# Kernel optimization log

Measured on AMD Instinct MI355X. Metric: run time of the kernel, lower is better.

## Reference

```python
import jax, jax.numpy as jnp
import numpy as np

L, B, N, D, H, DH, MLP = 4, 4, 2048, 512, 8, 64, 2048
EPS = 1e-5


def layer_norm(x, w, b):
    mu = jnp.mean(x, axis=-1, keepdims=True)
    var = jnp.mean(jnp.square(x - mu), axis=-1, keepdims=True)
    return (x - mu) * jax.lax.rsqrt(var + EPS) * w + b


def setup_inputs() -> dict:
    key = jax.random.key(0)
    ks = jax.random.split(key, 8)
    x = jax.random.normal(ks[0], (B, N, D), dtype=jnp.float32)
    # mask == 1.0 means blocked: triu(ones) - eye -> strict upper triangle
    mask = jnp.triu(jnp.ones((N, N), dtype=jnp.float32)) - jnp.eye(N, dtype=jnp.float32)
    s = 0.02
    return {
        "x": x,
        "mask": mask,
        "ln1_w": jnp.ones((L, D), jnp.float32),
        "ln1_b": jnp.zeros((L, D), jnp.float32),
        "w_qkv": jax.random.normal(ks[1], (L, D, 3 * H * DH), jnp.float32) * s,
        "w_out": jax.random.normal(ks[2], (L, H * DH, D), jnp.float32) * s,
        "b_out": jnp.zeros((L, D), jnp.float32),
        "ln2_w": jnp.ones((L, D), jnp.float32),
        "ln2_b": jnp.zeros((L, D), jnp.float32),
        "w1": jax.random.normal(ks[3], (L, D, MLP), jnp.float32) * s,
        "b1": jnp.zeros((L, MLP), jnp.float32),
        "w2": jax.random.normal(ks[4], (L, MLP, D), jnp.float32) * s,
        "b2": jnp.zeros((L, D), jnp.float32),
    }


def reference(x, mask, ln1_w, ln1_b, w_qkv, w_out, b_out, ln2_w, ln2_b, w1, b1, w2, b2):
    scale = DH ** (-0.5)
    blocked = (mask == 1.0)  # [N, N]
    for l in range(L):
        # --- masked self-attention (pre-norm) ---
        h = layer_norm(x, ln1_w[l], ln1_b[l])
        qkv = h @ w_qkv[l]                               # [B, N, 3*H*DH]
        q, k, v = jnp.split(qkv, 3, axis=-1)
        q = q.reshape(B, N, H, DH).transpose(0, 2, 1, 3)  # bhnd
        k = k.reshape(B, N, H, DH).transpose(0, 2, 1, 3)
        v = v.reshape(B, N, H, DH).transpose(0, 2, 1, 3)
        scores = jnp.einsum('bhnd,bhmd->bhnm', q, k) * scale
        scores = jnp.where(blocked, -jnp.inf, scores)
        att = jax.nn.softmax(scores, axis=-1)
        o = jnp.einsum('bhnm,bhmd->bhnd', att, v)
        o = o.transpose(0, 2, 1, 3).reshape(B, N, H * DH)
        x = x + (o @ w_out[l] + b_out[l])
        # --- GELU MLP (pre-norm) ---
        h2 = layer_norm(x, ln2_w[l], ln2_b[l])
        ff = jax.nn.gelu(h2 @ w1[l] + b1[l], approximate=False) @ w2[l] + b2[l]
        x = x + ff
    return x
```

## Files before the change

### kernel.cpp

```cpp
#include <hip/hip_runtime.h>
#include <math.h>

#define L 4
#define BATCH 4
#define N 2048
#define D 512
#define H 8
#define DH 64
#define MLPD 2048
#define M_ROWS (BATCH * N)
#define VTP 2064

using v8s = __attribute__((ext_vector_type(8))) short;
using v4f = __attribute__((ext_vector_type(4))) float;

__device__ inline short f2bf(float f) {
  union { float f; unsigned u; } v; v.f = f;
  unsigned r = v.u + 0x7FFFu + ((v.u >> 16) & 1u);
  return (short)(r >> 16);
}
__device__ inline unsigned pack2bf_t(float a, float b) {
  union { float f; unsigned u; } x, y; x.f = a; y.f = b;
  return (x.u >> 16) | (y.u & 0xFFFF0000u);
}

#define MFMA(a, b, c) __builtin_amdgcn_mfma_f32_16x16x32_bf16(a, b, c, 0, 0, 0)

__device__ __forceinline__ void gload_lds16(const void* g, void* l) {
  __builtin_amdgcn_global_load_lds((const __attribute__((address_space(1))) void*)g,
                                   (__attribute__((address_space(3))) void*)l, 16, 0, 0);
}

#define FENCE asm volatile("" ::: "memory")
#define BAR  do { FENCE; __builtin_amdgcn_s_barrier(); FENCE; } while (0)
#define VMW(n) asm volatile("s_waitcnt vmcnt(" #n ")" ::: "memory")

__global__ void copyf4_kernel(const float4* __restrict__ in, float4* __restrict__ out, int n) {
  int i = blockIdx.x * blockDim.x + threadIdx.x;
  if (i < n) out[i] = in[i];
}

__launch_bounds__(256)
__global__ void transpose_w_kernel(const float* __restrict__ src, short* __restrict__ dst,
                                   int R, int C) {
  __shared__ float tile[32][33];
  const size_t base = (size_t)blockIdx.z * R * C;
  const int c0 = blockIdx.x * 32, r0 = blockIdx.y * 32;
  const int tx = threadIdx.x & 31, ty = threadIdx.x >> 5;
  #pragma unroll
  for (int i = ty; i < 32; i += 8)
    tile[i][tx] = src[base + (size_t)(r0 + i) * C + c0 + tx];
  __syncthreads();
  #pragma unroll
  for (int i = ty; i < 32; i += 8)
    dst[base + (size_t)(c0 + i) * R + r0 + tx] = f2bf(tile[tx][i]);
}

__launch_bounds__(256)
__global__ void ln_kernel(const float* __restrict__ x, const float* __restrict__ w,
                          const float* __restrict__ b, short* __restrict__ out) {
  const int row = blockIdx.x * 4 + (threadIdx.x >> 6);
  const int lane = threadIdx.x & 63;
  const float* xr = x + (size_t)row * D;
  float4 a0 = *(const float4*)(xr + lane * 8);
  float4 a1 = *(const float4*)(xr + lane * 8 + 4);
  float v[8] = {a0.x, a0.y, a0.z, a0.w, a1.x, a1.y, a1.z, a1.w};
  float s = 0.f;
  #pragma unroll
  for (int j = 0; j < 8; ++j) s += v[j];
  #pragma unroll
  for (int m = 1; m < 64; m <<= 1) s += __shfl_xor(s, m, 64);
  const float mean = s * (1.0f / D);
  float q = 0.f;
  #pragma unroll
  for (int j = 0; j < 8; ++j) { float d = v[j] - mean; q += d * d; }
  #pragma unroll
  for (int m = 1; m < 64; m <<= 1) q += __shfl_xor(q, m, 64);
  const float rstd = rsqrtf(q * (1.0f / D) + 1e-5f);
  float4 w0 = *(const float4*)(w + lane * 8);
  float4 w1 = *(const float4*)(w + lane * 8 + 4);
  float4 b0 = *(const float4*)(b + lane * 8);
  float4 b1 = *(const float4*)(b + lane * 8 + 4);
  float wv[8] = {w0.x, w0.y, w0.z, w0.w, w1.x, w1.y, w1.z, w1.w};
  float bv[8] = {b0.x, b0.y, b0.z, b0.w, b1.x, b1.y, b1.z, b1.w};
  v8s r;
  #pragma unroll
  for (int j = 0; j < 8; ++j) r[j] = f2bf((v[j] - mean) * rstd * wv[j] + bv[j]);
  *(v8s*)(out + (size_t)row * D + lane * 8) = r;
}

template <int MODE, int NT>
__launch_bounds__(512, 2)
__global__ void gemm256_kernel(const short* __restrict__ A, const short* __restrict__ Bt,
                               const float* __restrict__ bias, void* __restrict__ Out,
                               int M, int Nc) {
  constexpr int K = NT * 64;
  __shared__ __align__(16) short Ah[4][128 * 64];
  __shared__ __align__(16) short Bh[4][128 * 64];
  const int tid = threadIdx.x, lane = tid & 63, w = tid >> 6;
  const int wr = w >> 2, wc = w & 3;
  const int r16 = lane & 15, g = lane >> 4;

  const int nxb = Nc >> 8;
  const int nyb = M >> 8;
  const int bid = (int)blockIdx.x;
  const int xcd = bid & 7, ii = bid >> 3;
  const int byi = xcd * (nyb >> 3) + ii / nxb;
  const int bxi = ii % nxb;
  const int m0 = byi << 8, n0 = bxi << 8;

  const int srow = lane >> 3;
  const int ssw = ((lane & 7) ^ srow) * 8;

  const short* Abase = A + (size_t)(m0 + srow) * K + ssw;
  const short* Bbase = Bt + (size_t)(n0 + srow) * K + ssw;

  auto STAGE_A = [&](int j) {
    if (j >= 2 * NT) return;
    const int slot = j & 3, k0 = (j >> 1) * 64, r0 = (j & 1) * 128;
    #pragma unroll
    for (int i = 0; i < 2; ++i) {
      const int rr = i * 64 + w * 8;
      gload_lds16(Abase + (size_t)(r0 + rr) * K + k0, (char*)&Ah[slot][0] + rr * 128);
    }
  };
  auto STAGE_B = [&](int j) {
    if (j >= 2 * NT) return;
    const int slot = j & 3, k0 = (j >> 1) * 64, c0 = (j & 1) * 128;
    #pragma unroll
    for (int i = 0; i < 2; ++i) {
      const int rr = i * 64 + w * 8;
      gload_lds16(Bbase + (size_t)(c0 + rr) * K + k0, (char*)&Bh[slot][0] + rr * 128);
    }
  };

  const int arow = wr * 64 + r16;
  const int brow = wc * 32 + r16;
  const int swz7 = r16 & 7;

  v8s ar[4][2], br0[2][2], br1[2][2];
  auto LDA = [&](int slot) {
    const char* base = (const char*)&Ah[slot][0];
    #pragma unroll
    for (int mf = 0; mf < 4; ++mf)
      #pragma unroll
      for (int kh = 0; kh < 2; ++kh)
        ar[mf][kh] = *(const v8s*)(base + (arow + mf * 16) * 128 + (((kh * 4 + g) ^ swz7) * 16));
  };
  auto LDB0 = [&](int slot) {
    const char* base = (const char*)&Bh[slot][0];
    #pragma unroll
    for (int nf = 0; nf < 2; ++nf)
      #pragma unroll
      for (int kh = 0; kh < 2; ++kh)
        br0[nf][kh] = *(const v8s*)(base + (brow + nf * 16) * 128 + (((kh * 4 + g) ^ swz7) * 16));
  };
  auto LDB1 = [&](int slot) {
    const char* base = (const char*)&Bh[slot][0];
    #pragma unroll
    for (int nf = 0; nf < 2; ++nf)
      #pragma unroll
      for (int kh = 0; kh < 2; ++kh)
        br1[nf][kh] = *(const v8s*)(base + (brow + nf * 16) * 128 + (((kh * 4 + g) ^ swz7) * 16));
  };

  v4f acc[2][2][4][2] = {};

#define MMA_Q(QM, QN, BR)                                                      \
  do {                                                                         \
    __builtin_amdgcn_s_setprio(1);                                             \
    _Pragma("unroll")                                                          \
    for (int kh = 0; kh < 2; ++kh)                                             \
      _Pragma("unroll")                                                        \
      for (int mf = 0; mf < 4; ++mf)                                           \
        _Pragma("unroll")                                                      \
        for (int nf = 0; nf < 2; ++nf)                                         \
          acc[QM][QN][mf][nf] = MFMA(ar[mf][kh], BR[nf][kh], acc[QM][QN][mf][nf]); \
    __builtin_amdgcn_s_setprio(0);                                             \
  } while (0)

  STAGE_A(0); STAGE_B(0); STAGE_B(1); STAGE_A(1); STAGE_A(2); STAGE_B(2); STAGE_B(3);
  VMW(6);
  BAR;

  auto KTILE = [&](int T, int sa) {
    LDA(sa); LDB0(sa);
    STAGE_A(2 * T + 3);
    BAR;
    MMA_Q(0, 0, br0);
    BAR;
    LDB1(sa + 1);
    BAR;
    MMA_Q(0, 1, br1);
    BAR;
    LDA(sa + 1);
    STAGE_A(2 * T + 4); STAGE_B(2 * T + 4);
    BAR;
    MMA_Q(1, 1, br1);
    BAR;
    STAGE_B(2 * T + 5);
    BAR;
    MMA_Q(1, 0, br0);
    VMW(4);
    BAR;
  };

  #pragma unroll
  for (int t2 = 0; t2 < NT / 2; ++t2) {
    KTILE(2 * t2, 0);
    KTILE(2 * t2 + 1, 2);
  }
#undef MMA_Q

  #pragma unroll
  for (int qm = 0; qm < 2; ++qm)
    #pragma unroll
    for (int mf = 0; mf < 4; ++mf) {
      const int row = m0 + qm * 128 + wr * 64 + mf * 16 + g * 4;
      #pragma unroll
      for (int qn = 0; qn < 2; ++qn)
        #pragma unroll
        for (int nf = 0; nf < 2; ++nf) {
          const int col = n0 + qn * 128 + wc * 32 + nf * 16 + r16;
          float bv = 0.0f;
          if constexpr (MODE == 1) bv = bias[col];
          #pragma unroll
          for (int r = 0; r < 4; ++r) {
            float val = acc[qm][qn][mf][nf][r] + bv;
            if constexpr (MODE == 1) {
              const float z = val * 0.70710678118f;
              const float az = fabsf(z);
              const float t = 1.0f / (1.0f + 0.3275911f * az);
              const float p =
                  0.254829592f +
                  t * (-0.284496736f + t * (1.421413741f + t * (-1.453152027f + t * 1.061405429f)));
              float er = 1.0f - p * t * __expf(-az * az);
              er = (z < 0.0f) ? -er : er;
              val = 0.5f * val * (1.0f + er);
            }
            ((short*)Out)[(size_t)(row + r) * Nc + col] = f2bf(val);
          }
        }
    }
}

template <int MODE, int BN>
__launch_bounds__(256)
__global__ void gemm128_kernel(const short* __restrict__ A, const short* __restrict__ Bt,
                               const float* __restrict__ bias, const float* __restrict__ Xres,
                               void* __restrict__ Out, int M, int Nc, int K) {
  constexpr int MR = (BN == 128) ? 4 : 2;
  __shared__ __align__(16) short As[2][128 * 64];
  __shared__ __align__(16) short Bs[2][BN * 64];
  const int tid = threadIdx.x;
  const int lane = tid & 63;
  const int w = tid >> 6;
  const int wr = (BN == 128) ? (w >> 1) : w;
  const int wc = (BN == 128) ? (w & 1) : 0;
  const int r16 = lane & 15, g = lane >> 4;

  const int nxb = Nc / BN;
  const int nyb = M >> 7;
  const int bid = (int)blockIdx.x;
  const int xcd = bid & 7;
  const int ii = bid >> 3;
  const int byi = xcd * (nyb >> 3) + ii / nxb;
  const int bxi = ii % nxb;
  const int m0 = byi * 128, n0 = bxi * BN;

  const int srow = lane >> 3;
  const int ssw = ((lane & 7) ^ srow) * 8;

  auto STAGE = [&](int buf, int k0) {
    #pragma unroll
    for (int j = 0; j < 4; ++j) {
      const int row = w * 32 + j * 8;
      gload_lds16(A + (size_t)(m0 + row + srow) * K + k0 + ssw,
                  (char*)&As[buf][0] + row * 128);
    }
    #pragma unroll
    for (int j = 0; j < BN / 32; ++j) {
      const int row = w * (BN / 4) + j * 8;
      gload_lds16(Bt + (size_t)(n0 + row + srow) * K + k0 + ssw,
                  (char*)&Bs[buf][0] + row * 128);
    }
  };

  v4f acc[MR][4] = {};

  STAGE(0, 0);
  __syncthreads();
  int cur = 0;
  for (int k0 = 0; k0 < K; k0 += 64) {
    if (k0 + 64 < K) STAGE(cur ^ 1, k0 + 64);
    v8s af[MR][2], bf[4][2];
    #pragma unroll
    for (int m = 0; m < MR; ++m) {
      const int row = wr * (MR * 16) + m * 16 + r16;
      #pragma unroll
      for (int kh = 0; kh < 2; ++kh)
        af[m][kh] = *(const v8s*)((const char*)&As[cur][0] + row * 128 +
                                  (((kh * 4 + g) ^ (row & 7)) * 16));
    }
    #pragma unroll
    for (int n = 0; n < 4; ++n) {
      const int row = wc * 64 + n * 16 + r16;
      #pragma unroll
      for (int kh = 0; kh < 2; ++kh)
        bf[n][kh] = *(const v8s*)((const char*)&Bs[cur][0] + row * 128 +
                                  (((kh * 4 + g) ^ (row & 7)) * 16));
    }
    #pragma unroll
    for (int kh = 0; kh < 2; ++kh)
      #pragma unroll
      for (int m = 0; m < MR; ++m)
        #pragma unroll
        for (int n = 0; n < 4; ++n)
          acc[m][n] = MFMA(af[m][kh], bf[n][kh], acc[m][n]);
    __syncthreads();
    cur ^= 1;
  }

  #pragma unroll
  for (int m = 0; m < MR; ++m) {
    const int row = m0 + wr * (MR * 16) + m * 16 + g * 4;
    #pragma unroll
    for (int n = 0; n < 4; ++n) {
      const int col = n0 + wc * 64 + n * 16 + r16;
      const float bv = bias ? bias[col] : 0.0f;
      #pragma unroll
      for (int r = 0; r < 4; ++r) {
        const size_t idx = (size_t)(row + r) * Nc + col;
        float val = acc[m][n][r] + bv;
        if constexpr (MODE == 0) {
          ((short*)Out)[idx] = f2bf(val);
        } else if constexpr (MODE == 1) {
          const float z = val * 0.70710678118f;
          const float az = fabsf(z);
          const float t = 1.0f / (1.0f + 0.3275911f * az);
          const float p =
              0.254829592f +
              t * (-0.284496736f + t * (1.421413741f + t * (-1.453152027f + t * 1.061405429f)));
          float er = 1.0f - p * t * __expf(-az * az);
          er = (z < 0.0f) ? -er : er;
          val = 0.5f * val * (1.0f + er);
          ((short*)Out)[idx] = f2bf(val);
        } else {
          ((float*)Out)[idx] = val + Xres[idx];
        }
      }
    }
  }
}

__launch_bounds__(256)
__global__ void kv_prep_kernel(const short* __restrict__ qkv, short* __restrict__ Vt) {
  __shared__ __align__(16) short tile[64][88];
  const int b = blockIdx.z, h = blockIdx.y, n0 = blockIdx.x * 64;
  const int tid = threadIdx.x;
  const int bh = b * H + h;
  const int row2 = tid >> 3, d0 = (tid & 7) * 8;
  #pragma unroll
  for (int i = 0; i < 2; ++i) {
    const int n = i * 32 + row2;
    const short* src = qkv + ((size_t)(b * N + n0 + n)) * 1536 + 1024 + h * 64 + d0;
    *(v8s*)&tile[n][d0] = *(const v8s*)src;
  }
  __syncthreads();
  const int dh = tid & 63, nc = (tid >> 6) * 16;
  #pragma unroll
  for (int j = 0; j < 2; ++j) {
    const int oc = nc + j * 8;
    const int base = (oc >> 5) * 32 + ((oc >> 3) & 3) * 4;
    v8s ov;
    #pragma unroll
    for (int e = 0; e < 4; ++e) ov[e] = tile[base + e][dh];
    #pragma unroll
    for (int e = 0; e < 4; ++e) ov[4 + e] = tile[base + 16 + e][dh];
    *(v8s*)(Vt + ((size_t)(bh * 64 + dh)) * VTP + n0 + oc) = ov;
  }
}

__launch_bounds__(256)
__global__ void attn_kernel(const short* __restrict__ qkv, const short* __restrict__ Vt,
                            short* __restrict__ o) {
  __shared__ __align__(16) short Ks[2][64 * 64];
  __shared__ __align__(16) short Vs[2][64 * 64];
  const int lin = (int)blockIdx.x;
  const int bh = ((lin >> 3) & 3) * 8 + (lin & 7);
  const int xl2 = 31 - (lin >> 5);
  const int b = bh >> 3, h = bh & 7;
  const int q0 = xl2 * 64;
  const int tid = threadIdx.x, lane = tid & 63, w = tid >> 6;
  const int r16 = lane & 15, g = lane >> 4;
  const int qw = q0 + w * 16;

  v8s qf0, qf1;
  {
    const size_t qbase = ((size_t)(b * N + qw + r16)) * 1536 + h * 64;
    qf0 = *(const v8s*)(qkv + qbase + g * 8);
    qf1 = *(const v8s*)(qkv + qbase + 32 + g * 8);
  }

  const short* vtb = Vt + (size_t)bh * 64 * VTP;

  const int srow = lane >> 3;
  const int ssw = ((lane & 7) ^ srow) * 8;

  v4f oacc[4] = {};
  float lsum = 0.f;
  const int tdiag = xl2;

  auto STAGE = [&](int buf, int t) {
    const int k0 = t * 64;
    #pragma unroll
    for (int j = 0; j < 2; ++j) {
      const int row = w * 16 + j * 8 + srow;
      gload_lds16(qkv + ((size_t)(b * N + k0 + row)) * 1536 + 512 + h * 64 + ssw,
                  (char*)&Ks[buf][0] + (w * 16 + j * 8) * 128);
      gload_lds16(vtb + (size_t)row * VTP + k0 + ssw,
                  (char*)&Vs[buf][0] + (w * 16 + j * 8) * 128);
    }
  };

  STAGE(0, 0);
  __syncthreads();
  int cur = 0;
  for (int t = 0; t <= tdiag; ++t) {
    if (t < tdiag) STAGE(cur ^ 1, t + 1);
    const int k0 = t * 64;
    const char* kb = (const char*)&Ks[cur][0];
    const char* vb = (const char*)&Vs[cur][0];

    v8s vf[4][2];
    #pragma unroll
    for (int a = 0; a < 4; ++a)
      #pragma unroll
      for (int c = 0; c < 2; ++c)
        vf[a][c] = *(const v8s*)(vb + (a * 16 + r16) * 128 + (((c * 4 + g) ^ (r16 & 7)) * 16));

    __builtin_amdgcn_s_setprio(1);
    v4f s[4];
    #pragma unroll
    for (int kt = 0; kt < 4; ++kt) {
      const int krow = (kt * 16 + r16) * 128;
      v8s kfa = *(const v8s*)(kb + krow + ((g ^ (r16 & 7)) * 16));
      v8s kfb = *(const v8s*)(kb + krow + (((4 + g) ^ (r16 & 7)) * 16));
      v4f ss = {};
      ss = MFMA(kfa, qf0, ss);
      ss = MFMA(kfb, qf1, ss);
      s[kt] = ss;
    }
    __builtin_amdgcn_s_setprio(0);

    const bool needmask = (t == tdiag);
    const int qrow = qw + r16;
    const int kbase = k0 + 4 * g;
    unsigned pw_[8];
    #pragma unroll
    for (int kt = 0; kt < 4; ++kt) {
      float e[4];
      #pragma unroll
      for (int r = 0; r < 4; ++r) {
        float v = s[kt][r] * 0.125f;
        if (needmask && (kbase + kt * 16 + r > qrow)) v = -3e38f;
        e[r] = __expf(v);
      }
      lsum += (e[0] + e[1]) + (e[2] + e[3]);
      pw_[kt * 2 + 0] = pack2bf_t(e[0], e[1]);
      pw_[kt * 2 + 1] = pack2bf_t(e[2], e[3]);
    }
    union PU { unsigned u[4]; v8s s8; };
    PU pa0, pa1;
    pa0.u[0] = pw_[0]; pa0.u[1] = pw_[1]; pa0.u[2] = pw_[2]; pa0.u[3] = pw_[3];
    pa1.u[0] = pw_[4]; pa1.u[1] = pw_[5]; pa1.u[2] = pw_[6]; pa1.u[3] = pw_[7];

    __builtin_amdgcn_s_setprio(1);
    #pragma unroll
    for (int dt = 0; dt < 4; ++dt) oacc[dt] = MFMA(pa0.s8, vf[dt][0], oacc[dt]);
    #pragma unroll
    for (int dt = 0; dt < 4; ++dt) oacc[dt] = MFMA(pa1.s8, vf[dt][1], oacc[dt]);
    __builtin_amdgcn_s_setprio(0);

    __syncthreads();
    cur ^= 1;
  }

  lsum += __shfl_xor(lsum, 16, 64);
  lsum += __shfl_xor(lsum, 32, 64);
  float ldiv[4];
  #pragma unroll
  for (int r = 0; r < 4; ++r) ldiv[r] = __shfl(lsum, g * 4 + r, 64);

  #pragma unroll
  for (int dt = 0; dt < 4; ++dt)
    #pragma unroll
    for (int r = 0; r < 4; ++r) {
      const float val = oacc[dt][r] / ldiv[r];
      o[((size_t)(b * N + qw + g * 4 + r)) * 512 + h * 64 + dt * 16 + r16] = f2bf(val);
    }
}

extern "C" void kernel_launch(void* const* d_in, const int* in_sizes, int n_in,
                              void* d_out, int out_size, void* d_ws, size_t ws_size,
                              hipStream_t stream) {
  const float* x_in  = (const float*)d_in[0];
  const float* ln1_w = (const float*)d_in[2];
  const float* ln1_b = (const float*)d_in[3];
  const float* w_qkv = (const float*)d_in[4];
  const float* w_out = (const float*)d_in[5];
  const float* b_out = (const float*)d_in[6];
  const float* ln2_w = (const float*)d_in[7];
  const float* ln2_b = (const float*)d_in[8];
  const float* w1    = (const float*)d_in[9];
  const float* b1    = (const float*)d_in[10];
  const float* w2    = (const float*)d_in[11];
  const float* b2    = (const float*)d_in[12];

  char* ws = (char*)d_ws;
  size_t off = 0;
  auto alloc = [&](size_t bytes) { char* p = ws + off; off += (bytes + 255) & ~(size_t)255; return p; };
  short* wqkvT = (short*)alloc((size_t)L * 1536 * 512 * 2);
  short* woutT = (short*)alloc((size_t)L * 512 * 512 * 2);
  short* w1T   = (short*)alloc((size_t)L * 512 * 2048 * 2);
  short* w2T   = (short*)alloc((size_t)L * 2048 * 512 * 2);
  short* hln   = (short*)alloc((size_t)M_ROWS * 512 * 2);
  short* big   = (short*)alloc((size_t)M_ROWS * 2048 * 2);
  short* oatt  = (short*)alloc((size_t)M_ROWS * 512 * 2);
  short* Vtg   = (short*)alloc((size_t)BATCH * H * 64 * VTP * 2);
  short* qkv = big;
  short* ff  = big;

  float* x = (float*)d_out;

  copyf4_kernel<<<4096, 256, 0, stream>>>((const float4*)x_in, (float4*)x, M_ROWS * D / 4);

  transpose_w_kernel<<<dim3(1536 / 32, 512 / 32, L), 256, 0, stream>>>(w_qkv, wqkvT, 512, 1536);
  transpose_w_kernel<<<dim3(512 / 32, 512 / 32, L), 256, 0, stream>>>(w_out, woutT, 512, 512);
  transpose_w_kernel<<<dim3(2048 / 32, 512 / 32, L), 256, 0, stream>>>(w1, w1T, 512, 2048);
  transpose_w_kernel<<<dim3(512 / 32, 2048 / 32, L), 256, 0, stream>>>(w2, w2T, 2048, 512);

  for (int l = 0; l < L; ++l) {
    ln_kernel<<<M_ROWS / 4, 256, 0, stream>>>(x, ln1_w + l * 512, ln1_b + l * 512, hln);
    gemm256_kernel<0, 8><<<dim3((1536 / 256) * (M_ROWS / 256)), 512, 0, stream>>>(
        hln, wqkvT + (size_t)l * 1536 * 512, nullptr, qkv, M_ROWS, 1536);
    kv_prep_kernel<<<dim3(N / 64, H, BATCH), 256, 0, stream>>>(qkv, Vtg);
    attn_kernel<<<dim3(1024), 256, 0, stream>>>(qkv, Vtg, oatt);
    gemm128_kernel<2, 64><<<dim3((512 / 64) * (M_ROWS / 128)), 256, 0, stream>>>(
        oatt, woutT + (size_t)l * 512 * 512, b_out + l * 512, x, x, M_ROWS, 512, 512);
    ln_kernel<<<M_ROWS / 4, 256, 0, stream>>>(x, ln2_w + l * 512, ln2_b + l * 512, hln);
    gemm256_kernel<1, 8><<<dim3((2048 / 256) * (M_ROWS / 256)), 512, 0, stream>>>(
        hln, w1T + (size_t)l * 512 * 2048, b1 + l * 2048, ff, M_ROWS, 2048);
    gemm128_kernel<2, 64><<<dim3((512 / 64) * (M_ROWS / 128)), 256, 0, stream>>>(
        ff, w2T + (size_t)l * 2048 * 512, b2 + l * 512, x, x, M_ROWS, 512, 2048);
  }
}
```

Before: 628.9 us.

## Switch attention to 32x32 MFMA tiles with 128-row query blocks

```diff
diff --git a/kernel.cpp b/kernel.cpp
--- a/kernel.cpp
+++ b/kernel.cpp
@@ -13,6 +13,7 @@
 
 using v8s = __attribute__((ext_vector_type(8))) short;
 using v4f = __attribute__((ext_vector_type(4))) float;
+using v16f = __attribute__((ext_vector_type(16))) float;
 
 __device__ inline short f2bf(float f) {
   union { float f; unsigned u; } v; v.f = f;
@@ -25,6 +26,7 @@
 }
 
 #define MFMA(a, b, c) __builtin_amdgcn_mfma_f32_16x16x32_bf16(a, b, c, 0, 0, 0)
+#define MFMA32(a, b, c) __builtin_amdgcn_mfma_f32_32x32x16_bf16(a, b, c, 0, 0, 0)
 
 __device__ __forceinline__ void gload_lds16(const void* g, void* l) {
   __builtin_amdgcn_global_load_lds((const __attribute__((address_space(1))) void*)g,
@@ -367,16 +369,16 @@
     *(v8s*)&tile[n][d0] = *(const v8s*)src;
   }
   __syncthreads();
-  const int dh = tid & 63, nc = (tid >> 6) * 16;
+  const int dh = tid & 63, nc2 = (tid >> 6) * 16;
   #pragma unroll
   for (int j = 0; j < 2; ++j) {
-    const int oc = nc + j * 8;
-    const int base = (oc >> 5) * 32 + ((oc >> 3) & 3) * 4;
+    const int oc = nc2 + j * 8;
+    const int base = (oc & ~8) + ((oc & 8) >> 1);
     v8s ov;
     #pragma unroll
     for (int e = 0; e < 4; ++e) ov[e] = tile[base + e][dh];
     #pragma unroll
-    for (int e = 0; e < 4; ++e) ov[4 + e] = tile[base + 16 + e][dh];
+    for (int e = 0; e < 4; ++e) ov[4 + e] = tile[base + 8 + e][dh];
     *(v8s*)(Vt + ((size_t)(bh * 64 + dh)) * VTP + n0 + oc) = ov;
   }
 }
@@ -387,118 +389,134 @@
   __shared__ __align__(16) short Ks[2][64 * 64];
   __shared__ __align__(16) short Vs[2][64 * 64];
   const int lin = (int)blockIdx.x;
-  const int bh = ((lin >> 3) & 3) * 8 + (lin & 7);
-  const int xl2 = 31 - (lin >> 5);
+  const int xcd = lin & 7;
+  const int kk = lin >> 3;
+  const int bh = (kk & 3) * 8 + xcd;
+  const int xl = (kk < 32) ? (15 - (kk >> 2)) : ((kk - 32) >> 2);
   const int b = bh >> 3, h = bh & 7;
-  const int q0 = xl2 * 64;
   const int tid = threadIdx.x, lane = tid & 63, w = tid >> 6;
-  const int r16 = lane & 15, g = lane >> 4;
-  const int qw = q0 + w * 16;
-
-  v8s qf0, qf1;
+  const int l31 = lane & 31, hi = lane >> 5, r7 = l31 & 7;
+  const int qb = xl * 128 + w * 32;
+
+  v8s qf[4];
   {
-    const size_t qbase = ((size_t)(b * N + qw + r16)) * 1536 + h * 64;
-    qf0 = *(const v8s*)(qkv + qbase + g * 8);
-    qf1 = *(const v8s*)(qkv + qbase + 32 + g * 8);
+    const short* qp = qkv + ((size_t)(b * N + qb + l31)) * 1536 + h * 64 + hi * 8;
+    #pragma unroll
+    for (int c = 0; c < 4; ++c) qf[c] = *(const v8s*)(qp + c * 16);
   }
 
   const short* vtb = Vt + (size_t)bh * 64 * VTP;
-
   const int srow = lane >> 3;
   const int ssw = ((lane & 7) ^ srow) * 8;
 
-  v4f oacc[4] = {};
-  float lsum = 0.f;
-  const int tdiag = xl2;
-
   auto STAGE = [&](int buf, int t) {
     const int k0 = t * 64;
     #pragma unroll
     for (int j = 0; j < 2; ++j) {
-      const int row = w * 16 + j * 8 + srow;
-      gload_lds16(qkv + ((size_t)(b * N + k0 + row)) * 1536 + 512 + h * 64 + ssw,
-                  (char*)&Ks[buf][0] + (w * 16 + j * 8) * 128);
-      gload_lds16(vtb + (size_t)row * VTP + k0 + ssw,
-                  (char*)&Vs[buf][0] + (w * 16 + j * 8) * 128);
-    }
-  };
+      const int row = w * 16 + j * 8;
+      gload_lds16(qkv + ((size_t)(b * N + k0 + row + srow)) * 1536 + 512 + h * 64 + ssw,
+                  (char*)&Ks[buf][0] + row * 128);
+      gload_lds16(vtb + (size_t)(row + srow) * VTP + k0 + ssw,
+                  (char*)&Vs[buf][0] + row * 128);
+    }
+  };
+
+  v16f o0 = {}, o1 = {};
+  float lsum = 0.f;
+  const int nt = 2 * xl + 2;
+  const int wlast = 2 * xl + (w >> 1);
 
   STAGE(0, 0);
   __syncthreads();
   int cur = 0;
-  for (int t = 0; t <= tdiag; ++t) {
-    if (t < tdiag) STAGE(cur ^ 1, t + 1);
-    const int k0 = t * 64;
-    const char* kb = (const char*)&Ks[cur][0];
-    const char* vb = (const char*)&Vs[cur][0];
-
-    v8s vf[4][2];
-    #pragma unroll
-    for (int a = 0; a < 4; ++a)
-      #pragma unroll
-      for (int c = 0; c < 2; ++c)
-        vf[a][c] = *(const v8s*)(vb + (a * 16 + r16) * 128 + (((c * 4 + g) ^ (r16 & 7)) * 16));
-
-    __builtin_amdgcn_s_setprio(1);
-    v4f s[4];
-    #pragma unroll
-    for (int kt = 0; kt < 4; ++kt) {
-      const int krow = (kt * 16 + r16) * 128;
-      v8s kfa = *(const v8s*)(kb + krow + ((g ^ (r16 & 7)) * 16));
-      v8s kfb = *(const v8s*)(kb + krow + (((4 + g) ^ (r16 & 7)) * 16));
-      v4f ss = {};
-      ss = MFMA(kfa, qf0, ss);
-      ss = MFMA(kfb, qf1, ss);
-      s[kt] = ss;
-    }
-    __builtin_amdgcn_s_setprio(0);
-
-    const bool needmask = (t == tdiag);
-    const int qrow = qw + r16;
-    const int kbase = k0 + 4 * g;
-    unsigned pw_[8];
-    #pragma unroll
-    for (int kt = 0; kt < 4; ++kt) {
-      float e[4];
-      #pragma unroll
-      for (int r = 0; r < 4; ++r) {
-        float v = s[kt][r] * 0.125f;
-        if (needmask && (kbase + kt * 16 + r > qrow)) v = -3e38f;
-        e[r] = __expf(v);
+  for (int t = 0; t < nt; ++t) {
+    if (t + 1 < nt) STAGE(cur ^ 1, t + 1);
+    if (t <= wlast) {
+      const char* kbp = (const char*)&Ks[cur][0];
+      const char* vbp = (const char*)&Vs[cur][0];
+      v8s kf0[4], kf1[4], vf0[4], vf1[4];
+      #pragma unroll
+      for (int c = 0; c < 4; ++c) {
+        const int off = ((2 * c + hi) ^ r7) * 16;
+        kf0[c] = *(const v8s*)(kbp + l31 * 128 + off);
+        kf1[c] = *(const v8s*)(kbp + (32 + l31) * 128 + off);
+        vf0[c] = *(const v8s*)(vbp + l31 * 128 + off);
+        vf1[c] = *(const v8s*)(vbp + (32 + l31) * 128 + off);
       }
-      lsum += (e[0] + e[1]) + (e[2] + e[3]);
-      pw_[kt * 2 + 0] = pack2bf_t(e[0], e[1]);
-      pw_[kt * 2 + 1] = pack2bf_t(e[2], e[3]);
-    }
-    union PU { unsigned u[4]; v8s s8; };
-    PU pa0, pa1;
-    pa0.u[0] = pw_[0]; pa0.u[1] = pw_[1]; pa0.u[2] = pw_[2]; pa0.u[3] = pw_[3];
-    pa1.u[0] = pw_[4]; pa1.u[1] = pw_[5]; pa1.u[2] = pw_[6]; pa1.u[3] = pw_[7];
-
-    __builtin_amdgcn_s_setprio(1);
-    #pragma unroll
-    for (int dt = 0; dt < 4; ++dt) oacc[dt] = MFMA(pa0.s8, vf[dt][0], oacc[dt]);
-    #pragma unroll
-    for (int dt = 0; dt < 4; ++dt) oacc[dt] = MFMA(pa1.s8, vf[dt][1], oacc[dt]);
-    __builtin_amdgcn_s_setprio(0);
-
+
+      __builtin_amdgcn_s_setprio(1);
+      v16f s0 = {}, s1 = {};
+      #pragma unroll
+      for (int c = 0; c < 4; ++c) s0 = MFMA32(kf0[c], qf[c], s0);
+      #pragma unroll
+      for (int c = 0; c < 4; ++c) s1 = MFMA32(kf1[c], qf[c], s1);
+      __builtin_amdgcn_s_setprio(0);
+
+      const int qrow = qb + l31;
+      const int kb0 = t * 64 + 4 * hi;
+      const bool msk = (t == wlast);
+      float e0[16], e1[16];
+      #pragma unroll
+      for (int r = 0; r < 16; ++r) {
+        const int key = kb0 + (r & 3) + 8 * (r >> 2);
+        float v0 = s0[r] * 0.125f;
+        float v1 = s1[r] * 0.125f;
+        if (msk) {
+          if (key > qrow) v0 = -3e38f;
+          if (key + 32 > qrow) v1 = -3e38f;
+        }
+        e0[r] = __expf(v0);
+        e1[r] = __expf(v1);
+        lsum += e0[r] + e1[r];
+      }
+      union PU { unsigned u[4]; v8s s8; };
+      PU pa[4];
+      #pragma unroll
+      for (int c = 0; c < 4; ++c) {
+        const int bs = 8 * (c & 1);
+        if (c < 2) {
+          pa[c].u[0] = pack2bf_t(e0[bs + 0], e0[bs + 1]);
+          pa[c].u[1] = pack2bf_t(e0[bs + 2], e0[bs + 3]);
+          pa[c].u[2] = pack2bf_t(e0[bs + 4], e0[bs + 5]);
+          pa[c].u[3] = pack2bf_t(e0[bs + 6], e0[bs + 7]);
+        } else {
+          pa[c].u[0] = pack2bf_t(e1[bs + 0], e1[bs + 1]);
+          pa[c].u[1] = pack2bf_t(e1[bs + 2], e1[bs + 3]);
+          pa[c].u[2] = pack2bf_t(e1[bs + 4], e1[bs + 5]);
+          pa[c].u[3] = pack2bf_t(e1[bs + 6], e1[bs + 7]);
+        }
+      }
+
+      __builtin_amdgcn_s_setprio(1);
+      #pragma unroll
+      for (int c = 0; c < 4; ++c) {
+        o0 = MFMA32(vf0[c], pa[c].s8, o0);
+        o1 = MFMA32(vf1[c], pa[c].s8, o1);
+      }
+      __builtin_amdgcn_s_setprio(0);
+    }
     __syncthreads();
     cur ^= 1;
   }
 
-  lsum += __shfl_xor(lsum, 16, 64);
   lsum += __shfl_xor(lsum, 32, 64);
-  float ldiv[4];
-  #pragma unroll
-  for (int r = 0; r < 4; ++r) ldiv[r] = __shfl(lsum, g * 4 + r, 64);
-
-  #pragma unroll
-  for (int dt = 0; dt < 4; ++dt)
-    #pragma unroll
-    for (int r = 0; r < 4; ++r) {
-      const float val = oacc[dt][r] / ldiv[r];
-      o[((size_t)(b * N + qw + g * 4 + r)) * 512 + h * 64 + dt * 16 + r16] = f2bf(val);
-    }
+  const float inv = 1.0f / lsum;
+  short* orow = o + ((size_t)(b * N + qb + l31)) * 512 + h * 64;
+  #pragma unroll
+  for (int m = 0; m < 4; ++m) {
+    const int dh = 8 * m + 4 * hi;
+    uint2 st0, st1;
+    st0.x = (unsigned)(unsigned short)f2bf(o0[4 * m + 0] * inv) |
+            ((unsigned)(unsigned short)f2bf(o0[4 * m + 1] * inv) << 16);
+    st0.y = (unsigned)(unsigned short)f2bf(o0[4 * m + 2] * inv) |
+            ((unsigned)(unsigned short)f2bf(o0[4 * m + 3] * inv) << 16);
+    *(uint2*)(orow + dh) = st0;
+    st1.x = (unsigned)(unsigned short)f2bf(o1[4 * m + 0] * inv) |
+            ((unsigned)(unsigned short)f2bf(o1[4 * m + 1] * inv) << 16);
+    st1.y = (unsigned)(unsigned short)f2bf(o1[4 * m + 2] * inv) |
+            ((unsigned)(unsigned short)f2bf(o1[4 * m + 3] * inv) << 16);
+    *(uint2*)(orow + 32 + dh) = st1;
+  }
 }
 
 extern "C" void kernel_launch(void* const* d_in, const int* in_sizes, int n_in,
@@ -545,7 +563,7 @@
     gemm256_kernel<0, 8><<<dim3((1536 / 256) * (M_ROWS / 256)), 512, 0, stream>>>(
         hln, wqkvT + (size_t)l * 1536 * 512, nullptr, qkv, M_ROWS, 1536);
     kv_prep_kernel<<<dim3(N / 64, H, BATCH), 256, 0, stream>>>(qkv, Vtg);
-    attn_kernel<<<dim3(1024), 256, 0, stream>>>(qkv, Vtg, oatt);
+    attn_kernel<<<dim3(512), 256, 0, stream>>>(qkv, Vtg, oatt);
     gemm128_kernel<2, 64><<<dim3((512 / 64) * (M_ROWS / 128)), 256, 0, stream>>>(
         oatt, woutT + (size_t)l * 512 * 512, b_out + l * 512, x, x, M_ROWS, 512, 512);
     ln_kernel<<<M_ROWS / 4, 256, 0, stream>>>(x, ln2_w + l * 512, ln2_b + l * 512, hln);
```

Result: slower. 710.1 us (+12.9%).

## Triple-buffer K tiles in attention and fold softmax scale into Q weights

Applied to the files above, without the earlier changes.

```diff
diff --git a/kernel.cpp b/kernel.cpp
--- a/kernel.cpp
+++ b/kernel.cpp
@@ -42,7 +42,7 @@
 
 __launch_bounds__(256)
 __global__ void transpose_w_kernel(const float* __restrict__ src, short* __restrict__ dst,
-                                   int R, int C) {
+                                   int R, int C, int qcols) {
   __shared__ float tile[32][33];
   const size_t base = (size_t)blockIdx.z * R * C;
   const int c0 = blockIdx.x * 32, r0 = blockIdx.y * 32;
@@ -52,8 +52,11 @@
     tile[i][tx] = src[base + (size_t)(r0 + i) * C + c0 + tx];
   __syncthreads();
   #pragma unroll
-  for (int i = ty; i < 32; i += 8)
-    dst[base + (size_t)(c0 + i) * R + r0 + tx] = f2bf(tile[tx][i]);
+  for (int i = ty; i < 32; i += 8) {
+    float val = tile[tx][i];
+    if (c0 + i < qcols) val *= 0.125f;
+    dst[base + (size_t)(c0 + i) * R + r0 + tx] = f2bf(val);
+  }
 }
 
 __launch_bounds__(256)
@@ -384,7 +387,7 @@
 __launch_bounds__(256)
 __global__ void attn_kernel(const short* __restrict__ qkv, const short* __restrict__ Vt,
                             short* __restrict__ o) {
-  __shared__ __align__(16) short Ks[2][64 * 64];
+  __shared__ __align__(16) short Ks[3][64 * 64];
   __shared__ __align__(16) short Vs[2][64 * 64];
   const int lin = (int)blockIdx.x;
   const int bh = ((lin >> 3) & 3) * 8 + (lin & 7);
@@ -411,26 +414,37 @@
   float lsum = 0.f;
   const int tdiag = xl2;
 
-  auto STAGE = [&](int buf, int t) {
-    const int k0 = t * 64;
+  auto STAGE_K = [&](int t) {
+    t = (t > tdiag) ? tdiag : t;
+    const int k0 = t * 64, buf = t % 3;
     #pragma unroll
     for (int j = 0; j < 2; ++j) {
-      const int row = w * 16 + j * 8 + srow;
-      gload_lds16(qkv + ((size_t)(b * N + k0 + row)) * 1536 + 512 + h * 64 + ssw,
-                  (char*)&Ks[buf][0] + (w * 16 + j * 8) * 128);
-      gload_lds16(vtb + (size_t)row * VTP + k0 + ssw,
-                  (char*)&Vs[buf][0] + (w * 16 + j * 8) * 128);
-    }
-  };
-
-  STAGE(0, 0);
-  __syncthreads();
-  int cur = 0;
+      const int row = w * 16 + j * 8;
+      gload_lds16(qkv + ((size_t)(b * N + k0 + row + srow)) * 1536 + 512 + h * 64 + ssw,
+                  (char*)&Ks[buf][0] + row * 128);
+    }
+  };
+  auto STAGE_V = [&](int t) {
+    t = (t > tdiag) ? tdiag : t;
+    const int k0 = t * 64, buf = t & 1;
+    #pragma unroll
+    for (int j = 0; j < 2; ++j) {
+      const int row = w * 16 + j * 8;
+      gload_lds16(vtb + (size_t)(row + srow) * VTP + k0 + ssw,
+                  (char*)&Vs[buf][0] + row * 128);
+    }
+  };
+
+  STAGE_K(0); STAGE_V(0); STAGE_K(1);
+
   for (int t = 0; t <= tdiag; ++t) {
-    if (t < tdiag) STAGE(cur ^ 1, t + 1);
-    const int k0 = t * 64;
-    const char* kb = (const char*)&Ks[cur][0];
-    const char* vb = (const char*)&Vs[cur][0];
+    VMW(2);
+    BAR;
+    STAGE_V(t + 1);
+    STAGE_K(t + 2);
+
+    const char* kb = (const char*)&Ks[t % 3][0];
+    const char* vb = (const char*)&Vs[t & 1][0];
 
     v8s vf[4][2];
     #pragma unroll
@@ -455,14 +469,14 @@
 
     const bool needmask = (t == tdiag);
     const int qrow = qw + r16;
-    const int kbase = k0 + 4 * g;
+    const int kbase = t * 64 + 4 * g;
     unsigned pw_[8];
     #pragma unroll
     for (int kt = 0; kt < 4; ++kt) {
       float e[4];
       #pragma unroll
       for (int r = 0; r < 4; ++r) {
-        float v = s[kt][r] * 0.125f;
+        float v = s[kt][r];
         if (needmask && (kbase + kt * 16 + r > qrow)) v = -3e38f;
         e[r] = __expf(v);
       }
@@ -481,9 +495,6 @@
     #pragma unroll
     for (int dt = 0; dt < 4; ++dt) oacc[dt] = MFMA(pa1.s8, vf[dt][1], oacc[dt]);
     __builtin_amdgcn_s_setprio(0);
-
-    __syncthreads();
-    cur ^= 1;
   }
 
   lsum += __shfl_xor(lsum, 16, 64);
@@ -535,10 +546,10 @@
 
   copyf4_kernel<<<4096, 256, 0, stream>>>((const float4*)x_in, (float4*)x, M_ROWS * D / 4);
 
-  transpose_w_kernel<<<dim3(1536 / 32, 512 / 32, L), 256, 0, stream>>>(w_qkv, wqkvT, 512, 1536);
-  transpose_w_kernel<<<dim3(512 / 32, 512 / 32, L), 256, 0, stream>>>(w_out, woutT, 512, 512);
-  transpose_w_kernel<<<dim3(2048 / 32, 512 / 32, L), 256, 0, stream>>>(w1, w1T, 512, 2048);
-  transpose_w_kernel<<<dim3(512 / 32, 2048 / 32, L), 256, 0, stream>>>(w2, w2T, 2048, 512);
+  transpose_w_kernel<<<dim3(1536 / 32, 512 / 32, L), 256, 0, stream>>>(w_qkv, wqkvT, 512, 1536, 512);
+  transpose_w_kernel<<<dim3(512 / 32, 512 / 32, L), 256, 0, stream>>>(w_out, woutT, 512, 512, 0);
+  transpose_w_kernel<<<dim3(2048 / 32, 512 / 32, L), 256, 0, stream>>>(w1, w1T, 512, 2048, 0);
+  transpose_w_kernel<<<dim3(512 / 32, 2048 / 32, L), 256, 0, stream>>>(w2, w2T, 2048, 512, 0);
 
   for (int l = 0; l < L; ++l) {
     ln_kernel<<<M_ROWS / 4, 256, 0, stream>>>(x, ln1_w + l * 512, ln1_b + l * 512, hln);
```

After: 627.5 us. About the same (-0.2%).
